# Performance work log

Measured on AMD Instinct MI355X. Metric: run time of the kernel, lower is better.

The kernel has to match this reference:

```python
import math
import jax, jax.numpy as jnp
import numpy as np

FS = 16000          # sample rate implied by undefined global `fs` in source
NFFT = 320          # win_len == frame_len
HOP = 160           # inc
C_SOUND = 340.0
ARRAY_DIS = 0.027


def _steering(F, n_ch, angle_deg):
    # h = conj(exp(-1j*2*pi*f_k * sensor * d * sin(theta)/c)) -> exp(+1j*...)
    f_k = np.arange(F) * (FS // NFFT)                      # integer bins * 50 Hz
    delay = np.arange(n_ch) * ARRAY_DIS * np.sin(angle_deg * np.pi / 180.0) / C_SOUND
    h = np.exp(1j * 2.0 * np.pi * f_k[:, None] * delay[None, :]).astype(np.complex64)
    return jnp.asarray(h)[..., None]                       # [F, C, 1]


def _stft(x, window):
    # x: [B, C, L] float32; torch.stft defaults: center=True, reflect pad
    pad = NFFT // 2
    xp = jnp.pad(x, ((0, 0), (0, 0), (pad, pad)), mode='reflect')
    T = 1 + (xp.shape[-1] - NFFT) // HOP
    idx = jnp.arange(T)[:, None] * HOP + jnp.arange(NFFT)[None, :]
    frames = xp[:, :, idx] * window                        # [B, C, T, NFFT]
    return jnp.fft.rfft(frames, axis=-1)                   # [B, C, T, F] complex64


def _istft(S):
    # S: [B, F, T] complex; torch.istft with default (rectangular) window
    frames = jnp.fft.irfft(jnp.moveaxis(S, 1, 2), n=NFFT, axis=-1)  # [B, T, NFFT]
    B, T, _ = frames.shape
    out_len = NFFT + HOP * (T - 1)
    idx = jnp.arange(T)[:, None] * HOP + jnp.arange(NFFT)[None, :]
    out = jnp.zeros((B, out_len), frames.dtype).at[:, idx].add(frames)
    wsum = jnp.zeros((out_len,), frames.dtype).at[idx.reshape(-1)].add(1.0)
    pad = NFFT // 2
    return (out / wsum)[:, pad:-pad]


def setup_inputs() -> dict:
    key = jax.random.key(0)
    B, L, C = 8, 160000, 4
    mc_wav = jax.random.normal(key, (B, L, C), dtype=jnp.float32)
    # torch.kaiser_window(320, periodic=True, beta=6)
    window = jnp.asarray(np.kaiser(NFFT + 1, 6.0)[:NFFT].astype(np.float32))
    return {"mc_wav": mc_wav, "window": window}


def reference(mc_wav, window):
    B, L, C = mc_wav.shape
    # pre-normalize: remove DC per channel, scale by per-batch global max-abs
    x = mc_wav - jnp.mean(mc_wav, axis=1, keepdims=True)
    x = x / jnp.max(jnp.abs(x), axis=(1, 2), keepdims=True)
    x = jnp.transpose(x, (0, 2, 1))                        # [B, C, L]

    S = _stft(x, window)                                   # [B, C, T, F]
    F = S.shape[-1]
    Xs = jnp.transpose(S, (2, 0, 3, 1))                    # [T, B, F, C] frames-first
    T = Xs.shape[0]

    h1 = _steering(F, C, -40.0)                            # [F, C, 1]
    h2 = _steering(F, C, 40.0)
    eye = jnp.eye(C, dtype=S.dtype)

    def beam(invR, h, X):
        num = jnp.einsum('bfcd,fdo->bfco', invR, h)        # invR @ h  [B,F,C,1]
        den = jnp.einsum('fco,bfco->bf', h.conj(), num)    # h^H invR h
        w = num[..., 0] / den[..., None]                   # [B, F, C]
        return jnp.einsum('bfc,bfc->bf', w.conj(), X)      # w^H X

    def step(RXX, inp):
        X, first = inp                                     # X: [B, F, C]
        outer = jnp.einsum('bfc,bfd->bfcd', X, X.conj())
        RXX = jnp.where(first, outer, 0.05 * RXX + 0.95 * outer)
        tr = jnp.trace(RXX, axis1=-2, axis2=-1)[..., None, None]
        invR = jnp.linalg.inv(RXX + (tr / C) * eye)        # diag-loaded inverse
        return RXX, (beam(invR, h1, X), beam(invR, h2, X))

    RXX0 = jnp.zeros((B, F, C, C), dtype=S.dtype)
    firsts = jnp.arange(T) == 0
    _, (s1, s2) = jax.lax.scan(step, RXX0, (Xs, firsts))

    S1 = jnp.transpose(s1, (1, 2, 0))                      # [B, F, T]
    S2 = jnp.transpose(s2, (1, 2, 0))
    return _istft(S1), _istft(S2)
```

## Files before the change

kernel.cpp:

```cpp
#include <hip/hip_runtime.h>
#include <hip/hip_bf16.h>
#include <math.h>

#define BB 8
#define LL 160000
#define CC 4
#define NFFT 320
#define HOP 160
#define FB 161
#define TT 1001
#define TP 1024
#define RBLK 128
#define PI_D 3.14159265358979323846
#define NPAD 160320

#define SCH 504
#define KWARM 4

#define GM 16016
#define KSEC 352
#define LDK 704
#define KT 11

typedef __attribute__((ext_vector_type(8))) short bf16x8;
typedef __attribute__((ext_vector_type(4))) float f32x4;

__device__ __forceinline__ void ldsdma16(const short* g, short* l){
    __builtin_amdgcn_global_load_lds((const __attribute__((address_space(1))) void*)g,
                                     (__attribute__((address_space(3))) void*)l, 16, 0, 0);
}

__device__ __forceinline__ float2 cmulf(float2 a, float2 b){
    return make_float2(a.x*b.x - a.y*b.y, a.x*b.y + a.y*b.x);
}
__device__ __forceinline__ float2 cmulcj(float2 a, float2 b){
    return make_float2(a.x*b.x + a.y*b.y, a.y*b.x - a.x*b.y);
}
__device__ __forceinline__ float2 cjmul(float2 a, float2 b){
    return make_float2(a.x*b.x + a.y*b.y, a.x*b.y - a.y*b.x);
}
__device__ __forceinline__ float2 csub(float2 a, float2 b){ return make_float2(a.x-b.x, a.y-b.y); }
__device__ __forceinline__ float2 cscale(float2 a, float s){ return make_float2(a.x*s, a.y*s); }
__device__ __forceinline__ float2 cdivf(float2 a, float2 b){
    float inv = 1.0f/(b.x*b.x + b.y*b.y);
    return make_float2((a.x*b.x + a.y*b.y)*inv, (a.y*b.x - a.x*b.y)*inv);
}
__device__ __forceinline__ short bf_hi(float v){
    __hip_bfloat16 h = __float2bfloat16(v);
    short s; __builtin_memcpy(&s, &h, 2); return s;
}
__device__ __forceinline__ short bf_lo(float v){
    __hip_bfloat16 h = __float2bfloat16(v);
    float r = v - __bfloat162float(h);
    __hip_bfloat16 l = __float2bfloat16(r);
    short s; __builtin_memcpy(&s, &l, 2); return s;
}

__global__ void k_gen(const float* __restrict__ win, float* __restrict__ htab,
                      short* __restrict__ Bts, short* __restrict__ Bt){
    int gid = blockIdx.x*256 + threadIdx.x;
    if (gid < 2*FB*CC){
        int i = gid;
        int c = i & 3;
        int k = (i >> 2) % FB;
        int m = i / (FB*CC);
        double coef = 2.0*PI_D*50.0*0.027*sin(40.0*PI_D/180.0)/340.0;
        double sgn = (m == 0) ? -1.0 : 1.0;
        double ph = sgn*coef*(double)k*(double)c;
        double s, c2;
        sincos(ph, &s, &c2);
        ((float2*)htab)[i] = make_float2((float)c2, (float)s);
        return;
    }
    gid -= 2*FB*CC;
    if (gid < 384*640){
        int col = gid / 640, kk = gid % 640;
        int n = (kk >= 320) ? kk - 320 : kk;
        int sec = (kk >= 320) ? 1 : 0;
        float v = 0.f;
        if (col < 2*FB){
            int k = col >> 1;
            double th = 2.0*PI_D*(double)k*(double)n/320.0;
            double s, co; sincos(th, &s, &co);
            double tw = (col & 1) ? -s : co;
            v = (float)((double)win[n]*tw);
        }
        Bts[gid] = sec ? bf_lo(v) : bf_hi(v);
        return;
    }
    gid -= 384*640;
    if (gid < NFFT*LDK){
        int n = gid / LDK, kk = gid % LDK;
        int sec = (kk >= KSEC) ? 1 : 0;
        int kk2 = kk - (sec ? KSEC : 0);
        float v = 0.f;
        if (kk2 < 2*FB){
            int bin = kk2 >> 1;
            double c = ((bin == 0 || bin == 160) ? 1.0 : 2.0) / 320.0;
            double th = 2.0*PI_D*(double)bin*(double)n/320.0;
            double s, co; sincos(th, &s, &co);
            v = (float)((kk2 & 1) ? -c*s : c*co);
        }
        Bt[(size_t)n*LDK + kk] = sec ? bf_lo(v) : bf_hi(v);
    }
}

__global__ __launch_bounds__(256) void k_stats1(const float* __restrict__ in, float* __restrict__ part){
    __shared__ float4 s4[256];
    __shared__ float4 mn4[256];
    __shared__ float4 mx4[256];
    int b = blockIdx.x / RBLK, chunk = blockIdx.x % RBLK;
    int tid = threadIdx.x;
    const float4* p = (const float4*)(in + (size_t)b*LL*CC);
    const int per = LL / RBLK;
    int start = chunk*per;
    float4 s  = make_float4(0.f,0.f,0.f,0.f);
    float4 mn = make_float4( 3.4e38f, 3.4e38f, 3.4e38f, 3.4e38f);
    float4 mx = make_float4(-3.4e38f,-3.4e38f,-3.4e38f,-3.4e38f);
    for (int i = start + tid; i < start + per; i += 256){
        float4 v = p[i];
        s.x += v.x; s.y += v.y; s.z += v.z; s.w += v.w;
        mn.x = fminf(mn.x, v.x); mn.y = fminf(mn.y, v.y); mn.z = fminf(mn.z, v.z); mn.w = fminf(mn.w, v.w);
        mx.x = fmaxf(mx.x, v.x); mx.y = fmaxf(mx.y, v.y); mx.z = fmaxf(mx.z, v.z); mx.w = fmaxf(mx.w, v.w);
    }
    s4[tid] = s; mn4[tid] = mn; mx4[tid] = mx;
    __syncthreads();
    for (int st = 128; st >= 1; st >>= 1){
        if (tid < st){
            float4 a = s4[tid], c = s4[tid+st];
            s4[tid] = make_float4(a.x+c.x, a.y+c.y, a.z+c.z, a.w+c.w);
            float4 d = mn4[tid], e = mn4[tid+st];
            mn4[tid] = make_float4(fminf(d.x,e.x), fminf(d.y,e.y), fminf(d.z,e.z), fminf(d.w,e.w));
            float4 f = mx4[tid], g = mx4[tid+st];
            mx4[tid] = make_float4(fmaxf(f.x,g.x), fmaxf(f.y,g.y), fmaxf(f.z,g.z), fmaxf(f.w,g.w));
        }
        __syncthreads();
    }
    if (tid == 0){
        float* dst = part + (size_t)(b*RBLK + chunk)*12;
        float4 a = s4[0], d = mn4[0], f = mx4[0];
        dst[0]=a.x; dst[1]=a.y; dst[2]=a.z; dst[3]=a.w;
        dst[4]=d.x; dst[5]=d.y; dst[6]=d.z; dst[7]=d.w;
        dst[8]=f.x; dst[9]=f.y; dst[10]=f.z; dst[11]=f.w;
    }
}

__global__ __launch_bounds__(128) void k_stats2(const float* __restrict__ part,
                                                float* __restrict__ mean, float* __restrict__ invmax){
    __shared__ float4 s4[128];
    __shared__ float4 mn4[128];
    __shared__ float4 mx4[128];
    int b = blockIdx.x, tid = threadIdx.x;
    const float* src = part + (size_t)(b*RBLK + tid)*12;
    s4[tid]  = make_float4(src[0], src[1], src[2], src[3]);
    mn4[tid] = make_float4(src[4], src[5], src[6], src[7]);
    mx4[tid] = make_float4(src[8], src[9], src[10], src[11]);
    __syncthreads();
    for (int st = 64; st >= 1; st >>= 1){
        if (tid < st){
            float4 a = s4[tid], c = s4[tid+st];
            s4[tid] = make_float4(a.x+c.x, a.y+c.y, a.z+c.z, a.w+c.w);
            float4 d = mn4[tid], e = mn4[tid+st];
            mn4[tid] = make_float4(fminf(d.x,e.x), fminf(d.y,e.y), fminf(d.z,e.z), fminf(d.w,e.w));
            float4 f = mx4[tid], g = mx4[tid+st];
            mx4[tid] = make_float4(fmaxf(f.x,g.x), fmaxf(f.y,g.y), fmaxf(f.z,g.z), fmaxf(f.w,g.w));
        }
        __syncthreads();
    }
    if (tid == 0){
        float4 sum = s4[0], mn = mn4[0], mx = mx4[0];
        float m0 = sum.x*(1.0f/LL), m1 = sum.y*(1.0f/LL), m2 = sum.z*(1.0f/LL), m3 = sum.w*(1.0f/LL);
        mean[b*4+0]=m0; mean[b*4+1]=m1; mean[b*4+2]=m2; mean[b*4+3]=m3;
        float a0 = fmaxf(mx.x - m0, m0 - mn.x);
        float a1 = fmaxf(mx.y - m1, m1 - mn.y);
        float a2 = fmaxf(mx.z - m2, m2 - mn.z);
        float a3 = fmaxf(mx.w - m3, m3 - mn.w);
        invmax[b] = 1.0f / fmaxf(fmaxf(a0, a1), fmaxf(a2, a3));
    }
}

__global__ __launch_bounds__(256) void k_anorm(const float* __restrict__ in,
        const float* __restrict__ mean, const float* __restrict__ invmax,
        short* __restrict__ Ahi, short* __restrict__ Alo){
    int gid = blockIdx.x*256 + threadIdx.x;
    if (gid >= BB*CC*(NPAD/8)) return;
    int p8 = gid % (NPAD/8);
    int bc = gid / (NPAD/8);
    int b = bc >> 2;
    float mc = mean[bc];
    float iv = invmax[b];
    const float* px = in + (size_t)b*LL*CC + (bc & 3);
    bf16x8 h8, l8;
    #pragma unroll
    for (int j = 0; j < 8; ++j){
        int p = p8*8 + j - 160;
        int m2 = p < 0 ? -p : (p >= LL ? 2*LL - 2 - p : p);
        float v = (px[(size_t)m2*CC] - mc) * iv;
        __hip_bfloat16 h = __float2bfloat16(v);
        float r = v - __bfloat162float(h);
        __hip_bfloat16 l = __float2bfloat16(r);
        short hs, ls; __builtin_memcpy(&hs, &h, 2); __builtin_memcpy(&ls, &l, 2);
        h8[j] = hs; l8[j] = ls;
    }
    size_t o = (size_t)bc*NPAD + (size_t)p8*8;
    *(bf16x8*)&Ahi[o] = h8;
    *(bf16x8*)&Alo[o] = l8;
}

__global__ __launch_bounds__(256) void k_gstft(const short* __restrict__ Ahi, const short* __restrict__ Alo,
        const short* __restrict__ Bts, float* __restrict__ S){
    __shared__ short stage[16384];
    float* Ct = (float*)stage;
    int tid = threadIdx.x;
    int row0 = blockIdx.x*64;
    int col0 = blockIdx.y*64;
    int b  = row0 >> 12;
    int t0 = (row0 & 4095) >> 2;
    if (t0 >= TT) return;
    int wave = tid >> 6, lane = tid & 63;
    int wm = wave >> 1, wn = wave & 1;
    int l15 = lane & 15, quad = lane >> 4;
    int rowS  = wave*16 + (lane >> 2);
    int chunk = (lane & 3) ^ ((lane >> 3) & 3);
    int tls = t0 + (rowS >> 2); if (tls >= TT) tls = TT - 1;
    size_t gao = (size_t)(b*4 + (rowS & 3))*NPAD + (size_t)tls*160 + chunk*8;
    const short* gAh = Ahi + gao;
    const short* gAl = Alo + gao;
    const short* gB  = Bts + (size_t)(col0 + rowS)*640 + chunk*8;
    short* lA = stage + wave*512;
    int sw  = (l15 >> 1) & 3;
    int c0r = (quad ^ sw) * 8;
    int ra0 = (wm*32 + l15)*32 + c0r;
    int ra1 = (wm*32 + 16 + l15)*32 + c0r;
    int rb0 = (wn*32 + l15)*32 + c0r;
    int rb1 = (wn*32 + 16 + l15)*32 + c0r;
    f32x4 acc00 = {0.f,0.f,0.f,0.f}, acc01 = acc00, acc10 = acc00, acc11 = acc00;

    #define STG(kt_, off_) do{ \
        ldsdma16(gAh + (kt_)*32,       lA + (off_));        \
        ldsdma16(gAl + (kt_)*32,       lA + (off_) + 2048); \
        ldsdma16(gB  + (kt_)*32,       lA + (off_) + 4096); \
        ldsdma16(gB  + (kt_)*32 + 320, lA + (off_) + 6144); \
    }while(0)

    STG(0, 0);
    STG(1, 8192);
    #pragma unroll
    for (int kt = 0; kt < 10; ++kt){
        int offc = (kt & 1) ? 8192 : 0;
        if (kt < 9) asm volatile("s_waitcnt vmcnt(4)" ::: "memory");
        else        asm volatile("s_waitcnt vmcnt(0)" ::: "memory");
        __builtin_amdgcn_s_barrier();
        bf16x8 a0h = *(bf16x8*)&stage[offc + ra0];
        bf16x8 a1h = *(bf16x8*)&stage[offc + ra1];
        bf16x8 a0l = *(bf16x8*)&stage[offc + 2048 + ra0];
        bf16x8 a1l = *(bf16x8*)&stage[offc + 2048 + ra1];
        bf16x8 b0h = *(bf16x8*)&stage[offc + 4096 + rb0];
        bf16x8 b1h = *(bf16x8*)&stage[offc + 4096 + rb1];
        bf16x8 b0l = *(bf16x8*)&stage[offc + 6144 + rb0];
        bf16x8 b1l = *(bf16x8*)&stage[offc + 6144 + rb1];
        asm volatile("s_waitcnt lgkmcnt(0)" ::: "memory");
        __builtin_amdgcn_sched_barrier(0);
        __builtin_amdgcn_s_barrier();
        if (kt < 8) STG(kt+2, offc);
        acc00 = __builtin_amdgcn_mfma_f32_16x16x32_bf16(a0h, b0h, acc00, 0, 0, 0);
        acc01 = __builtin_amdgcn_mfma_f32_16x16x32_bf16(a0h, b1h, acc01, 0, 0, 0);
        acc10 = __builtin_amdgcn_mfma_f32_16x16x32_bf16(a1h, b0h, acc10, 0, 0, 0);
        acc11 = __builtin_amdgcn_mfma_f32_16x16x32_bf16(a1h, b1h, acc11, 0, 0, 0);
        acc00 = __builtin_amdgcn_mfma_f32_16x16x32_bf16(a0l, b0h, acc00, 0, 0, 0);
        acc01 = __builtin_amdgcn_mfma_f32_16x16x32_bf16(a0l, b1h, acc01, 0, 0, 0);
        acc10 = __builtin_amdgcn_mfma_f32_16x16x32_bf16(a1l, b0h, acc10, 0, 0, 0);
        acc11 = __builtin_amdgcn_mfma_f32_16x16x32_bf16(a1l, b1h, acc11, 0, 0, 0);
        acc00 = __builtin_amdgcn_mfma_f32_16x16x32_bf16(a0h, b0l, acc00, 0, 0, 0);
        acc01 = __builtin_amdgcn_mfma_f32_16x16x32_bf16(a0h, b1l, acc01, 0, 0, 0);
        acc10 = __builtin_amdgcn_mfma_f32_16x16x32_bf16(a1h, b0l, acc10, 0, 0, 0);
        acc11 = __builtin_amdgcn_mfma_f32_16x16x32_bf16(a1h, b1l, acc11, 0, 0, 0);
    }
    #undef STG
    #pragma unroll
    for (int r = 0; r < 4; ++r){
        int rl = wm*32 + quad*4 + r;
        Ct[rl*66 + wn*32 + l15]           = acc00[r];
        Ct[rl*66 + wn*32 + l15 + 16]      = acc01[r];
        Ct[(rl+16)*66 + wn*32 + l15]      = acc10[r];
        Ct[(rl+16)*66 + wn*32 + l15 + 16] = acc11[r];
    }
    __syncthreads();
    int tl = tid & 15, h = (tid >> 4) & 1, kq = tid >> 5;
    int t = t0 + tl;
    if (t < TT){
        float4* S4 = (float4*)S;
        for (int kk = kq; kk < 32; kk += 8){
            int kg = (col0 >> 1) + kk;
            if (kg < FB){
                float2 e0 = *(float2*)&Ct[(tl*4 + 2*h)*66 + 2*kk];
                float2 e1 = *(float2*)&Ct[(tl*4 + 2*h + 1)*66 + 2*kk];
                S4[((size_t)(b*FB + kg)*TT + t)*2 + h] = make_float4(e0.x, e0.y, e1.x, e1.y);
            }
        }
    }
}

#define UPD(first) do{ \
    float aa = (first) ? 0.f : 0.05f; float wg = (first) ? 1.f : 0.95f; \
    float y0x=wg*x0.x, y0y=wg*x0.y, y1x=wg*x1.x, y1y=wg*x1.y; \
    float y2x=wg*x2.x, y2y=wg*x2.y, y3x=wg*x3.x, y3y=wg*x3.y; \
    d0 = aa*d0 + y0x*x0.x + y0y*x0.y; \
    d1 = aa*d1 + y1x*x1.x + y1y*x1.y; \
    d2 = aa*d2 + y2x*x2.x + y2y*x2.y; \
    d3 = aa*d3 + y3x*x3.x + y3y*x3.y; \
    r10.x = aa*r10.x + y1x*x0.x + y1y*x0.y;  r10.y = aa*r10.y + y1y*x0.x - y1x*x0.y; \
    r20.x = aa*r20.x + y2x*x0.x + y2y*x0.y;  r20.y = aa*r20.y + y2y*x0.x - y2x*x0.y; \
    r30.x = aa*r30.x + y3x*x0.x + y3y*x0.y;  r30.y = aa*r30.y + y3y*x0.x - y3x*x0.y; \
    r21.x = aa*r21.x + y2x*x1.x + y2y*x1.y;  r21.y = aa*r21.y + y2y*x1.x - y2x*x1.y; \
    r31.x = aa*r31.x + y3x*x1.x + y3y*x1.y;  r31.y = aa*r31.y + y3y*x1.x - y3x*x1.y; \
    r32.x = aa*r32.x + y3x*x2.x + y3y*x2.y;  r32.y = aa*r32.y + y3y*x2.x - y3x*x2.y; \
}while(0)

__global__ __launch_bounds__(512) void k_scan(const float* __restrict__ S, const float* __restrict__ htab,
                      float* __restrict__ S1, float* __restrict__ S2){
    __shared__ float4 tile[1008];
    int bid = blockIdx.x;
    int half = bid & 1;
    int bf = bid >> 1;
    int f  = bf % FB;
    int tid = threadIdx.x;
    int tbase = half*SCH;
    int te  = tbase + SCH; if (te > TT) te = TT;
    int nst = 2*(te - tbase);
    const float4* Sg = (const float4*)S + (size_t)bf*TT*2;
    const float4* Sp = Sg + (size_t)tbase*2;
    for (int i = tid; i < nst; i += 512)
        tile[i ^ ((i>>4)&7)] = Sp[i];
    __syncthreads();
    float2 out1, out2;
    int t0 = tbase + tid;
    bool act = (tid < SCH) && (t0 < TT);
    if (act){
        const float2* hp = (const float2*)htab;
        float2 ha0 = hp[f*4+0], ha1 = hp[f*4+1], ha2 = hp[f*4+2], ha3 = hp[f*4+3];
        float2 hb0 = hp[(FB+f)*4+0], hb1 = hp[(FB+f)*4+1], hb2 = hp[(FB+f)*4+2], hb3 = hp[(FB+f)*4+3];
        float d0=0,d1=0,d2=0,d3=0;
        float2 r10={0,0}, r20={0,0}, r30={0,0}, r21={0,0}, r31={0,0}, r32={0,0};
        int ts = t0 - KWARM; if (ts < 0) ts = 0;
        for (int tau = ts; tau < t0; ++tau){
            float4 v0, v1;
            if (tau >= tbase){
                int i0 = 2*(tau - tbase);
                v0 = tile[i0 ^ ((i0>>4)&7)];
                v1 = tile[(i0+1) ^ ((i0>>4)&7)];
            } else {
                v0 = Sg[2*tau];
                v1 = Sg[2*tau + 1];
            }
            float2 x0 = make_float2(v0.x, v0.y), x1 = make_float2(v0.z, v0.w);
            float2 x2 = make_float2(v1.x, v1.y), x3 = make_float2(v1.z, v1.w);
            UPD(tau == 0);
        }
        {
            int t = t0;
            int i0 = 2*(t - tbase);
            float4 v0 = tile[i0 ^ ((i0>>4)&7)];
            float4 v1 = tile[(i0+1) ^ ((i0>>4)&7)];
            float2 x0 = make_float2(v0.x, v0.y), x1 = make_float2(v0.z, v0.w);
            float2 x2 = make_float2(v1.x, v1.y), x3 = make_float2(v1.z, v1.w);
            UPD(t == 0);
            float trc = d0 + d1 + d2 + d3;
            float lam = trc * 0.25f;
            float e0 = d0 + lam, e1 = d1 + lam, e2 = d2 + lam, e3 = d3 + lam;
            float detP = e0*e1 - (r10.x*r10.x + r10.y*r10.y);
            float2 w00 = csub(cscale(r20, e1), cmulf(r10, r21));
            float2 w01 = csub(cscale(r30, e1), cmulf(r10, r31));
            float2 w10 = csub(cscale(r21, e0), cjmul(r10, r20));
            float2 w11 = csub(cscale(r31, e0), cjmul(r10, r30));
            float2 va = cjmul(r30, w00), vb = cjmul(r31, w10);
            float2 V10 = make_float2(va.x + vb.x, -(va.y + vb.y));
            float reV00 = r20.x*w00.x + r20.y*w00.y + r21.x*w10.x + r21.y*w10.y;
            float reV11 = r30.x*w01.x + r30.y*w01.y + r31.x*w11.x + r31.y*w11.y;
            float t00 = detP*e2 - reV00;
            float t11 = detP*e3 - reV11;
            float2 t10 = csub(cscale(r32, detP), V10);
            float detT = t00*t11 - (t10.x*t10.x + t10.y*t10.y);
            #pragma unroll
            for (int m = 0; m < 2; ++m){
                float2 h0 = m ? hb0 : ha0;
                float2 h1 = m ? hb1 : ha1;
                float2 h2 = m ? hb2 : ha2;
                float2 h3 = m ? hb3 : ha3;
                float2 g0 = csub(cscale(h0, e1), cjmul(r10, h1));
                float2 g1 = csub(cscale(h1, e0), cmulf(r10, h0));
                float2 ta = cmulf(r20, g0), tb = cmulf(r21, g1);
                float2 hh0 = make_float2(detP*h2.x - ta.x - tb.x, detP*h2.y - ta.y - tb.y);
                ta = cmulf(r30, g0); tb = cmulf(r31, g1);
                float2 hh1 = make_float2(detP*h3.x - ta.x - tb.x, detP*h3.y - ta.y - tb.y);
                float2 y20 = csub(cscale(hh0, t11), cjmul(t10, hh1));
                float2 y21 = csub(cscale(hh1, t00), cmulf(t10, hh0));
                float2 u20 = cscale(y20, detP), u21 = cscale(y21, detP);
                ta = cmulcj(y20, r20); tb = cmulcj(y21, r30);
                float2 q0 = make_float2(detT*h0.x - ta.x - tb.x, detT*h0.y - ta.y - tb.y);
                ta = cmulcj(y20, r21); tb = cmulcj(y21, r31);
                float2 q1 = make_float2(detT*h1.x - ta.x - tb.x, detT*h1.y - ta.y - tb.y);
                float2 u10 = csub(cscale(q0, e1), cjmul(r10, q1));
                float2 u11 = csub(cscale(q1, e0), cmulf(r10, q0));
                float2 den = cjmul(h0, u10), tmp;
                tmp = cjmul(h1, u11); den.x += tmp.x; den.y += tmp.y;
                tmp = cjmul(h2, u20); den.x += tmp.x; den.y += tmp.y;
                tmp = cjmul(h3, u21); den.x += tmp.x; den.y += tmp.y;
                float2 num = cjmul(u10, x0);
                tmp = cjmul(u11, x1); num.x += tmp.x; num.y += tmp.y;
                tmp = cjmul(u20, x2); num.x += tmp.x; num.y += tmp.y;
                tmp = cjmul(u21, x3); num.x += tmp.x; num.y += tmp.y;
                float2 s = cdivf(num, make_float2(den.x, -den.y));
                if (m) out2 = s; else out1 = s;
            }
        }
    }
    __syncthreads();
    float2* o1 = (float2*)tile;
    float2* o2 = ((float2*)tile) + 528;
    if (act){
        int lt = t0 - tbase;
        int iw = lt ^ ((lt>>3)&7);
        o1[iw] = out1;
        o2[iw] = out2;
    }
    __syncthreads();
    int nout = te - tbase;
    float2* S1g = (float2*)S1 + (size_t)bf*TT + tbase;
    float2* S2g = (float2*)S2 + (size_t)bf*TT + tbase;
    for (int i = tid; i < nout; i += 512){
        int ir = i ^ ((i>>3)&7);
        S1g[i] = o1[ir];
        S2g[i] = o2[ir];
    }
}

__global__ __launch_bounds__(256) void k_pack(const float* __restrict__ S1, const float* __restrict__ S2,
                                              short* __restrict__ A){
    __shared__ short tile[32*708];
    int bid = blockIdx.x;
    int tb = bid & 31, rb = bid >> 5;
    int t0 = tb*32;
    int beam = rb >> 3, b = rb & 7;
    const float2* Sp = (const float2*)(beam ? S2 : S1) + (size_t)b*FB*TT;
    int tid = threadIdx.x;
    for (int idx = tid; idx < 32*176; idx += 256){
        int bin = idx >> 5, tq = idx & 31;
        int t = t0 + tq;
        float2 s = make_float2(0.f, 0.f);
        if (bin < FB && t < TT) s = Sp[(size_t)bin*TT + t];
        int c0 = 2*bin;
        tile[tq*708 + c0]            = bf_hi(s.x);
        tile[tq*708 + c0 + 1]        = bf_hi(s.y);
        tile[tq*708 + KSEC + c0]     = bf_lo(s.x);
        tile[tq*708 + KSEC + c0 + 1] = bf_lo(s.y);
    }
    __syncthreads();
    for (int idx = tid; idx < 32*176; idx += 256){
        int tq = idx / 176, k4 = idx % 176;
        int t = t0 + tq;
        if (t < TT)
            *(short4*)&A[(size_t)(rb*TT + t)*LDK + k4*4] = *(short4*)&tile[tq*708 + k4*4];
    }
}

__global__ __launch_bounds__(256) void k_gemm(const short* __restrict__ A, const short* __restrict__ Bt,
                                              float* __restrict__ C){
    __shared__ short sb2[8192];
    int tid = threadIdx.x;
    int row0 = blockIdx.x * 64;
    int col0 = blockIdx.y * 64;
    int wave = tid >> 6, lane = tid & 63;
    int wm = wave >> 1, wn = wave & 1;
    int l15 = lane & 15, quad = lane >> 4;
    int rowS  = wave*16 + (lane >> 2);
    int chunk = (lane & 3) ^ ((lane >> 3) & 3);
    int grS = row0 + rowS; if (grS >= GM) grS = GM - 1;
    const short* gA = A  + (size_t)grS*LDK + chunk*8;
    const short* gB = Bt + (size_t)(col0 + rowS)*LDK + chunk*8;
    short* lA = sb2 + wave*512;
    int sw  = (l15 >> 1) & 3;
    int c0r = (quad ^ sw) * 8;
    int ra0 = (wm*32 + l15)*32 + c0r;
    int ra1 = (wm*32 + 16 + l15)*32 + c0r;
    int rb0 = (wn*32 + l15)*32 + c0r;
    int rb1 = (wn*32 + 16 + l15)*32 + c0r;
    f32x4 acc00 = {0.f,0.f,0.f,0.f}, acc01 = acc00, acc10 = acc00, acc11 = acc00;

    #define KOF(s_, ka_, kb_) { int sg_ = ((s_) >= 22) ? 2 : ((s_) >= 11) ? 1 : 0; \
        int kt_ = (s_) - sg_*11; \
        ka_ = ((sg_ == 1) ? KSEC : 0) + kt_*32; \
        kb_ = ((sg_ == 2) ? KSEC : 0) + kt_*32; }
    #define STG2(s_, off_) do{ int ka_, kb_; KOF(s_, ka_, kb_); \
        ldsdma16(gA + ka_, lA + (off_));        \
        ldsdma16(gB + kb_, lA + (off_) + 2048); \
    }while(0)

    STG2(0, 0);
    STG2(1, 4096);
    #pragma unroll
    for (int s = 0; s < 33; ++s){
        int offc = (s & 1) ? 4096 : 0;
        if (s < 32) asm volatile("s_waitcnt vmcnt(2)" ::: "memory");
        else        asm volatile("s_waitcnt vmcnt(0)" ::: "memory");
        __builtin_amdgcn_s_barrier();
        bf16x8 a0 = *(bf16x8*)&sb2[offc + ra0];
        bf16x8 a1 = *(bf16x8*)&sb2[offc + ra1];
        bf16x8 b0 = *(bf16x8*)&sb2[offc + 2048 + rb0];
        bf16x8 b1 = *(bf16x8*)&sb2[offc + 2048 + rb1];
        asm volatile("s_waitcnt lgkmcnt(0)" ::: "memory");
        __builtin_amdgcn_sched_barrier(0);
        __builtin_amdgcn_s_barrier();
        if (s < 31) STG2(s+2, offc);
        acc00 = __builtin_amdgcn_mfma_f32_16x16x32_bf16(a0, b0, acc00, 0, 0, 0);
        acc01 = __builtin_amdgcn_mfma_f32_16x16x32_bf16(a0, b1, acc01, 0, 0, 0);
        acc10 = __builtin_amdgcn_mfma_f32_16x16x32_bf16(a1, b0, acc10, 0, 0, 0);
        acc11 = __builtin_amdgcn_mfma_f32_16x16x32_bf16(a1, b1, acc11, 0, 0, 0);
    }
    #undef STG2
    #undef KOF
    for (int r = 0; r < 4; ++r){
        int orow0 = row0 + wm*32 + quad*4 + r;
        int ocol0 = col0 + wn*32 + l15;
        if (orow0 < GM){
            C[(size_t)orow0*NFFT + ocol0]      = acc00[r];
            C[(size_t)orow0*NFFT + ocol0 + 16] = acc01[r];
        }
        if (orow0 + 16 < GM){
            C[(size_t)(orow0+16)*NFFT + ocol0]      = acc10[r];
            C[(size_t)(orow0+16)*NFFT + ocol0 + 16] = acc11[r];
        }
    }
}

__global__ __launch_bounds__(256) void k_ola(const float* __restrict__ frames, float* __restrict__ out){
    int gid = blockIdx.x*256 + threadIdx.x;
    if (gid >= 2*BB*(LL/4)) return;
    int o4 = (gid % (LL/4))*4;
    int rb = gid / (LL/4);
    int i  = o4 + HOP;
    int t1 = i / HOP;
    int r  = i - t1*HOP;
    const float4* fb = (const float4*)(frames + (size_t)rb*TT*NFFT);
    float4 a = fb[(t1*NFFT + r) >> 2];
    float4 b = fb[((t1-1)*NFFT + r + HOP) >> 2];
    ((float4*)out)[gid] = make_float4(0.5f*(a.x+b.x), 0.5f*(a.y+b.y), 0.5f*(a.z+b.z), 0.5f*(a.w+b.w));
}

extern "C" void kernel_launch(void* const* d_in, const int* in_sizes, int n_in,
                              void* d_out, int out_size, void* d_ws, size_t ws_size,
                              hipStream_t stream){
    const float* in  = (const float*)d_in[0];
    const float* win = (const float*)d_in[1];
    float* ws = (float*)d_ws;
    float* mean   = ws;
    float* invmax = ws + 32;
    float* htab   = ws + 48;
    float* S1     = ws + 3072;
    size_t nS1 = (size_t)2*BB*FB*TT;
    float* S2 = S1 + nS1;
    float* S  = S2 + nS1;
    float* part = S1;
    short* Ahi = (short*)S1;
    short* Alo = Ahi + (size_t)BB*CC*NPAD;
    short* Bts = (short*)d_out;
    short* Bt  = (short*)((float*)d_out + 131072);
    short* A  = (short*)S;
    float* frames = S1;

    int ngen = 2*FB*CC + 384*640 + NFFT*LDK;
    k_gen<<<dim3((ngen + 255)/256), dim3(256), 0, stream>>>(win, htab, Bts, Bt);
    k_stats1<<<dim3(BB*RBLK), dim3(256), 0, stream>>>(in, part);
    k_stats2<<<dim3(BB), dim3(128), 0, stream>>>(part, mean, invmax);
    k_anorm<<<dim3((BB*CC*(NPAD/8) + 255)/256), dim3(256), 0, stream>>>(in, mean, invmax, Ahi, Alo);
    k_gstft<<<dim3(BB*TP*CC/64, 6), dim3(256), 0, stream>>>(Ahi, Alo, Bts, S);
    k_scan<<<dim3(2*BB*FB), dim3(512), 0, stream>>>(S, htab, S1, S2);
    k_pack<<<dim3(512), dim3(256), 0, stream>>>(S1, S2, A);
    k_gemm<<<dim3((GM + 63)/64, NFFT/64), dim3(256), 0, stream>>>(A, Bt, frames);
    k_ola<<<dim3((2*BB*(LL/4) + 255)/256), dim3(256), 0, stream>>>(frames, (float*)d_out);
}
```

Measured before the change: 220.4 us.

## Enlarge STFT and iSTFT GEMM tiles to 128x128 with 512-thread blocks

Both MFMA GEMM kernels move from 64x64 tiles with 4 waves to 128x128 tiles with 8 waves, so each wave now computes a 32x64 sub-tile with 8 accumulators. This is meant to raise operand reuse per LDS load and cut global traffic. The STFT epilogue drops the LDS transpose and writes straight from registers using lane shuffles, and the layout of S changes to split channel pairs into separate planes, so the scan kernel's loads are rewritten to match. The cost is more registers per thread, fewer blocks, and wasted work on padded columns (320 is not a multiple of 128), which needs bounds guards.

```diff
diff --git a/kernel.cpp b/kernel.cpp
--- a/kernel.cpp
+++ b/kernel.cpp
@@ -207,16 +207,14 @@
     *(bf16x8*)&Alo[o] = l8;
 }
 
-__global__ __launch_bounds__(256) void k_gstft(const short* __restrict__ Ahi, const short* __restrict__ Alo,
+__global__ __launch_bounds__(512, 4) void k_gstft(const short* __restrict__ Ahi, const short* __restrict__ Alo,
         const short* __restrict__ Bts, float* __restrict__ S){
-    __shared__ short stage[16384];
-    float* Ct = (float*)stage;
+    __shared__ short stage[32768];
     int tid = threadIdx.x;
-    int row0 = blockIdx.x*64;
-    int col0 = blockIdx.y*64;
+    int row0 = blockIdx.x*128;
+    int col0 = blockIdx.y*128;
     int b  = row0 >> 12;
     int t0 = (row0 & 4095) >> 2;
-    if (t0 >= TT) return;
     int wave = tid >> 6, lane = tid & 63;
     int wm = wave >> 1, wn = wave & 1;
     int l15 = lane & 15, quad = lane >> 4;
@@ -231,74 +229,87 @@
     int sw  = (l15 >> 1) & 3;
     int c0r = (quad ^ sw) * 8;
     int ra0 = (wm*32 + l15)*32 + c0r;
-    int ra1 = (wm*32 + 16 + l15)*32 + c0r;
-    int rb0 = (wn*32 + l15)*32 + c0r;
-    int rb1 = (wn*32 + 16 + l15)*32 + c0r;
-    f32x4 acc00 = {0.f,0.f,0.f,0.f}, acc01 = acc00, acc10 = acc00, acc11 = acc00;
+    int rb0 = (wn*64 + l15)*32 + c0r;
+    f32x4 c00 = {0.f,0.f,0.f,0.f}, c01 = c00, c02 = c00, c03 = c00;
+    f32x4 c10 = c00, c11 = c00, c12 = c00, c13 = c00;
 
     #define STG(kt_, off_) do{ \
-        ldsdma16(gAh + (kt_)*32,       lA + (off_));        \
-        ldsdma16(gAl + (kt_)*32,       lA + (off_) + 2048); \
-        ldsdma16(gB  + (kt_)*32,       lA + (off_) + 4096); \
-        ldsdma16(gB  + (kt_)*32 + 320, lA + (off_) + 6144); \
+        ldsdma16(gAh + (kt_)*32,       lA + (off_));         \
+        ldsdma16(gAl + (kt_)*32,       lA + (off_) + 4096);  \
+        ldsdma16(gB  + (kt_)*32,       lA + (off_) + 8192);  \
+        ldsdma16(gB  + (kt_)*32 + 320, lA + (off_) + 12288); \
     }while(0)
 
     STG(0, 0);
-    STG(1, 8192);
+    STG(1, 16384);
     #pragma unroll
     for (int kt = 0; kt < 10; ++kt){
-        int offc = (kt & 1) ? 8192 : 0;
+        int offc = (kt & 1) ? 16384 : 0;
         if (kt < 9) asm volatile("s_waitcnt vmcnt(4)" ::: "memory");
         else        asm volatile("s_waitcnt vmcnt(0)" ::: "memory");
         __builtin_amdgcn_s_barrier();
         bf16x8 a0h = *(bf16x8*)&stage[offc + ra0];
-        bf16x8 a1h = *(bf16x8*)&stage[offc + ra1];
-        bf16x8 a0l = *(bf16x8*)&stage[offc + 2048 + ra0];
-        bf16x8 a1l = *(bf16x8*)&stage[offc + 2048 + ra1];
-        bf16x8 b0h = *(bf16x8*)&stage[offc + 4096 + rb0];
-        bf16x8 b1h = *(bf16x8*)&stage[offc + 4096 + rb1];
-        bf16x8 b0l = *(bf16x8*)&stage[offc + 6144 + rb0];
-        bf16x8 b1l = *(bf16x8*)&stage[offc + 6144 + rb1];
+        bf16x8 a1h = *(bf16x8*)&stage[offc + ra0 + 512];
+        bf16x8 a0l = *(bf16x8*)&stage[offc + 4096 + ra0];
+        bf16x8 a1l = *(bf16x8*)&stage[offc + 4096 + ra0 + 512];
+        bf16x8 b0h = *(bf16x8*)&stage[offc + 8192 + rb0];
+        bf16x8 b1h = *(bf16x8*)&stage[offc + 8192 + rb0 + 512];
+        bf16x8 b2h = *(bf16x8*)&stage[offc + 8192 + rb0 + 1024];
+        bf16x8 b3h = *(bf16x8*)&stage[offc + 8192 + rb0 + 1536];
+        bf16x8 b0l = *(bf16x8*)&stage[offc + 12288 + rb0];
+        bf16x8 b1l = *(bf16x8*)&stage[offc + 12288 + rb0 + 512];
+        bf16x8 b2l = *(bf16x8*)&stage[offc + 12288 + rb0 + 1024];
+        bf16x8 b3l = *(bf16x8*)&stage[offc + 12288 + rb0 + 1536];
         asm volatile("s_waitcnt lgkmcnt(0)" ::: "memory");
         __builtin_amdgcn_sched_barrier(0);
         __builtin_amdgcn_s_barrier();
         if (kt < 8) STG(kt+2, offc);
-        acc00 = __builtin_amdgcn_mfma_f32_16x16x32_bf16(a0h, b0h, acc00, 0, 0, 0);
-        acc01 = __builtin_amdgcn_mfma_f32_16x16x32_bf16(a0h, b1h, acc01, 0, 0, 0);
-        acc10 = __builtin_amdgcn_mfma_f32_16x16x32_bf16(a1h, b0h, acc10, 0, 0, 0);
-        acc11 = __builtin_amdgcn_mfma_f32_16x16x32_bf16(a1h, b1h, acc11, 0, 0, 0);
-        acc00 = __builtin_amdgcn_mfma_f32_16x16x32_bf16(a0l, b0h, acc00, 0, 0, 0);
-        acc01 = __builtin_amdgcn_mfma_f32_16x16x32_bf16(a0l, b1h, acc01, 0, 0, 0);
-        acc10 = __builtin_amdgcn_mfma_f32_16x16x32_bf16(a1l, b0h, acc10, 0, 0, 0);
-        acc11 = __builtin_amdgcn_mfma_f32_16x16x32_bf16(a1l, b1h, acc11, 0, 0, 0);
-        acc00 = __builtin_amdgcn_mfma_f32_16x16x32_bf16(a0h, b0l, acc00, 0, 0, 0);
-        acc01 = __builtin_amdgcn_mfma_f32_16x16x32_bf16(a0h, b1l, acc01, 0, 0, 0);
-        acc10 = __builtin_amdgcn_mfma_f32_16x16x32_bf16(a1h, b0l, acc10, 0, 0, 0);
-        acc11 = __builtin_amdgcn_mfma_f32_16x16x32_bf16(a1h, b1l, acc11, 0, 0, 0);
+        c00 = __builtin_amdgcn_mfma_f32_16x16x32_bf16(a0h, b0h, c00, 0, 0, 0);
+        c01 = __builtin_amdgcn_mfma_f32_16x16x32_bf16(a0h, b1h, c01, 0, 0, 0);
+        c02 = __builtin_amdgcn_mfma_f32_16x16x32_bf16(a0h, b2h, c02, 0, 0, 0);
+        c03 = __builtin_amdgcn_mfma_f32_16x16x32_bf16(a0h, b3h, c03, 0, 0, 0);
+        c10 = __builtin_amdgcn_mfma_f32_16x16x32_bf16(a1h, b0h, c10, 0, 0, 0);
+        c11 = __builtin_amdgcn_mfma_f32_16x16x32_bf16(a1h, b1h, c11, 0, 0, 0);
+        c12 = __builtin_amdgcn_mfma_f32_16x16x32_bf16(a1h, b2h, c12, 0, 0, 0);
+        c13 = __builtin_amdgcn_mfma_f32_16x16x32_bf16(a1h, b3h, c13, 0, 0, 0);
+        c00 = __builtin_amdgcn_mfma_f32_16x16x32_bf16(a0l, b0h, c00, 0, 0, 0);
+        c01 = __builtin_amdgcn_mfma_f32_16x16x32_bf16(a0l, b1h, c01, 0, 0, 0);
+        c02 = __builtin_amdgcn_mfma_f32_16x16x32_bf16(a0l, b2h, c02, 0, 0, 0);
+        c03 = __builtin_amdgcn_mfma_f32_16x16x32_bf16(a0l, b3h, c03, 0, 0, 0);
+        c10 = __builtin_amdgcn_mfma_f32_16x16x32_bf16(a1l, b0h, c10, 0, 0, 0);
+        c11 = __builtin_amdgcn_mfma_f32_16x16x32_bf16(a1l, b1h, c11, 0, 0, 0);
+        c12 = __builtin_amdgcn_mfma_f32_16x16x32_bf16(a1l, b2h, c12, 0, 0, 0);
+        c13 = __builtin_amdgcn_mfma_f32_16x16x32_bf16(a1l, b3h, c13, 0, 0, 0);
+        c00 = __builtin_amdgcn_mfma_f32_16x16x32_bf16(a0h, b0l, c00, 0, 0, 0);
+        c01 = __builtin_amdgcn_mfma_f32_16x16x32_bf16(a0h, b1l, c01, 0, 0, 0);
+        c02 = __builtin_amdgcn_mfma_f32_16x16x32_bf16(a0h, b2l, c02, 0, 0, 0);
+        c03 = __builtin_amdgcn_mfma_f32_16x16x32_bf16(a0h, b3l, c03, 0, 0, 0);
+        c10 = __builtin_amdgcn_mfma_f32_16x16x32_bf16(a1h, b0l, c10, 0, 0, 0);
+        c11 = __builtin_amdgcn_mfma_f32_16x16x32_bf16(a1h, b1l, c11, 0, 0, 0);
+        c12 = __builtin_amdgcn_mfma_f32_16x16x32_bf16(a1h, b2l, c12, 0, 0, 0);
+        c13 = __builtin_amdgcn_mfma_f32_16x16x32_bf16(a1h, b3l, c13, 0, 0, 0);
     }
     #undef STG
-    #pragma unroll
-    for (int r = 0; r < 4; ++r){
-        int rl = wm*32 + quad*4 + r;
-        Ct[rl*66 + wn*32 + l15]           = acc00[r];
-        Ct[rl*66 + wn*32 + l15 + 16]      = acc01[r];
-        Ct[(rl+16)*66 + wn*32 + l15]      = acc10[r];
-        Ct[(rl+16)*66 + wn*32 + l15 + 16] = acc11[r];
-    }
-    __syncthreads();
-    int tl = tid & 15, h = (tid >> 4) & 1, kq = tid >> 5;
-    int t = t0 + tl;
-    if (t < TT){
-        float4* S4 = (float4*)S;
-        for (int kk = kq; kk < 32; kk += 8){
-            int kg = (col0 >> 1) + kk;
-            if (kg < FB){
-                float2 e0 = *(float2*)&Ct[(tl*4 + 2*h)*66 + 2*kk];
-                float2 e1 = *(float2*)&Ct[(tl*4 + 2*h + 1)*66 + 2*kk];
-                S4[((size_t)(b*FB + kg)*TT + t)*2 + h] = make_float4(e0.x, e0.y, e1.x, e1.y);
-            }
-        }
-    }
+    int tq  = t0 + wm*8 + quad;
+    int kgb = (col0 >> 1) + wn*32 + (l15 >> 1);
+    int h   = l15 & 1;
+    float4* S4 = (float4*)S;
+    #define EPI(cf, i_, j_) do{ \
+        int t = tq + 4*(i_); \
+        int kg = kgb + 8*(j_); \
+        if (t < TT && kg < FB){ \
+            float p0 = __shfl_xor(cf[0], 1); \
+            float p1 = __shfl_xor(cf[1], 1); \
+            float p2 = __shfl_xor(cf[2], 1); \
+            float p3 = __shfl_xor(cf[3], 1); \
+            float4 v = h ? make_float4(p2, cf[2], p3, cf[3]) \
+                         : make_float4(cf[0], p0, cf[1], p1); \
+            S4[((size_t)((b*FB + kg)*2 + h))*TT + t] = v; \
+        } \
+    }while(0)
+    EPI(c00, 0, 0); EPI(c01, 0, 1); EPI(c02, 0, 2); EPI(c03, 0, 3);
+    EPI(c10, 1, 0); EPI(c11, 1, 1); EPI(c12, 1, 2); EPI(c13, 1, 3);
+    #undef EPI
 }
 
 #define UPD(first) do{ \
@@ -328,10 +339,12 @@
     int tbase = half*SCH;
     int te  = tbase + SCH; if (te > TT) te = TT;
     int nst = 2*(te - tbase);
-    const float4* Sg = (const float4*)S + (size_t)bf*TT*2;
-    const float4* Sp = Sg + (size_t)tbase*2;
-    for (int i = tid; i < nst; i += 512)
-        tile[i ^ ((i>>4)&7)] = Sp[i];
+    const float4* P0 = (const float4*)S + (size_t)(bf*2)*TT;
+    const float4* P1 = P0 + TT;
+    for (int i = tid; i < nst; i += 512){
+        int tt = tbase + (i >> 1);
+        tile[i ^ ((i>>4)&7)] = (i & 1) ? P1[tt] : P0[tt];
+    }
     __syncthreads();
     float2 out1, out2;
     int t0 = tbase + tid;
@@ -350,8 +363,8 @@
                 v0 = tile[i0 ^ ((i0>>4)&7)];
                 v1 = tile[(i0+1) ^ ((i0>>4)&7)];
             } else {
-                v0 = Sg[2*tau];
-                v1 = Sg[2*tau + 1];
+                v0 = P0[tau];
+                v1 = P1[tau];
             }
             float2 x0 = make_float2(v0.x, v0.y), x1 = make_float2(v0.z, v0.w);
             float2 x2 = make_float2(v1.x, v1.y), x3 = make_float2(v1.z, v1.w);
@@ -464,28 +477,28 @@
     }
 }
 
-__global__ __launch_bounds__(256) void k_gemm(const short* __restrict__ A, const short* __restrict__ Bt,
-                                              float* __restrict__ C){
-    __shared__ short sb2[8192];
+__global__ __launch_bounds__(512, 4) void k_gemm(const short* __restrict__ A, const short* __restrict__ Bt,
+                                                 float* __restrict__ C){
+    __shared__ short sb2[16384];
     int tid = threadIdx.x;
-    int row0 = blockIdx.x * 64;
-    int col0 = blockIdx.y * 64;
+    int row0 = blockIdx.x * 128;
+    int col0 = blockIdx.y * 128;
     int wave = tid >> 6, lane = tid & 63;
     int wm = wave >> 1, wn = wave & 1;
     int l15 = lane & 15, quad = lane >> 4;
     int rowS  = wave*16 + (lane >> 2);
     int chunk = (lane & 3) ^ ((lane >> 3) & 3);
     int grS = row0 + rowS; if (grS >= GM) grS = GM - 1;
+    int grB = col0 + rowS; if (grB >= NFFT) grB = NFFT - 1;
     const short* gA = A  + (size_t)grS*LDK + chunk*8;
-    const short* gB = Bt + (size_t)(col0 + rowS)*LDK + chunk*8;
+    const short* gB = Bt + (size_t)grB*LDK + chunk*8;
     short* lA = sb2 + wave*512;
     int sw  = (l15 >> 1) & 3;
     int c0r = (quad ^ sw) * 8;
     int ra0 = (wm*32 + l15)*32 + c0r;
-    int ra1 = (wm*32 + 16 + l15)*32 + c0r;
-    int rb0 = (wn*32 + l15)*32 + c0r;
-    int rb1 = (wn*32 + 16 + l15)*32 + c0r;
-    f32x4 acc00 = {0.f,0.f,0.f,0.f}, acc01 = acc00, acc10 = acc00, acc11 = acc00;
+    int rb0 = (wn*64 + l15)*32 + c0r;
+    f32x4 c00 = {0.f,0.f,0.f,0.f}, c01 = c00, c02 = c00, c03 = c00;
+    f32x4 c10 = c00, c11 = c00, c12 = c00, c13 = c00;
 
     #define KOF(s_, ka_, kb_) { int sg_ = ((s_) >= 22) ? 2 : ((s_) >= 11) ? 1 : 0; \
         int kt_ = (s_) - sg_*11; \
@@ -493,42 +506,53 @@
         kb_ = ((sg_ == 2) ? KSEC : 0) + kt_*32; }
     #define STG2(s_, off_) do{ int ka_, kb_; KOF(s_, ka_, kb_); \
         ldsdma16(gA + ka_, lA + (off_));        \
-        ldsdma16(gB + kb_, lA + (off_) + 2048); \
+        ldsdma16(gB + kb_, lA + (off_) + 4096); \
     }while(0)
 
     STG2(0, 0);
-    STG2(1, 4096);
+    STG2(1, 8192);
     #pragma unroll
     for (int s = 0; s < 33; ++s){
-        int offc = (s & 1) ? 4096 : 0;
+        int offc = (s & 1) ? 8192 : 0;
         if (s < 32) asm volatile("s_waitcnt vmcnt(2)" ::: "memory");
         else        asm volatile("s_waitcnt vmcnt(0)" ::: "memory");
         __builtin_amdgcn_s_barrier();
         bf16x8 a0 = *(bf16x8*)&sb2[offc + ra0];
-        bf16x8 a1 = *(bf16x8*)&sb2[offc + ra1];
-        bf16x8 b0 = *(bf16x8*)&sb2[offc + 2048 + rb0];
-        bf16x8 b1 = *(bf16x8*)&sb2[offc + 2048 + rb1];
+        bf16x8 a1 = *(bf16x8*)&sb2[offc + ra0 + 512];
+        bf16x8 b0 = *(bf16x8*)&sb2[offc + 4096 + rb0];
+        bf16x8 b1 = *(bf16x8*)&sb2[offc + 4096 + rb0 + 512];
+        bf16x8 b2 = *(bf16x8*)&sb2[offc + 4096 + rb0 + 1024];
+        bf16x8 b3 = *(bf16x8*)&sb2[offc + 4096 + rb0 + 1536];
         asm volatile("s_waitcnt lgkmcnt(0)" ::: "memory");
         __builtin_amdgcn_sched_barrier(0);
         __builtin_amdgcn_s_barrier();
         if (s < 31) STG2(s+2, offc);
-        acc00 = __builtin_amdgcn_mfma_f32_16x16x32_bf16(a0, b0, acc00, 0, 0, 0);
-        acc01 = __builtin_amdgcn_mfma_f32_16x16x32_bf16(a0, b1, acc01, 0, 0, 0);
-        acc10 = __builtin_amdgcn_mfma_f32_16x16x32_bf16(a1, b0, acc10, 0, 0, 0);
-        acc11 = __builtin_amdgcn_mfma_f32_16x16x32_bf16(a1, b1, acc11, 0, 0, 0);
+        c00 = __builtin_amdgcn_mfma_f32_16x16x32_bf16(a0, b0, c00, 0, 0, 0);
+        c01 = __builtin_amdgcn_mfma_f32_16x16x32_bf16(a0, b1, c01, 0, 0, 0);
+        c02 = __builtin_amdgcn_mfma_f32_16x16x32_bf16(a0, b2, c02, 0, 0, 0);
+        c03 = __builtin_amdgcn_mfma_f32_16x16x32_bf16(a0, b3, c03, 0, 0, 0);
+        c10 = __builtin_amdgcn_mfma_f32_16x16x32_bf16(a1, b0, c10, 0, 0, 0);
+        c11 = __builtin_amdgcn_mfma_f32_16x16x32_bf16(a1, b1, c11, 0, 0, 0);
+        c12 = __builtin_amdgcn_mfma_f32_16x16x32_bf16(a1, b2, c12, 0, 0, 0);
+        c13 = __builtin_amdgcn_mfma_f32_16x16x32_bf16(a1, b3, c13, 0, 0, 0);
     }
     #undef STG2
     #undef KOF
+    #pragma unroll
     for (int r = 0; r < 4; ++r){
         int orow0 = row0 + wm*32 + quad*4 + r;
-        int ocol0 = col0 + wn*32 + l15;
+        int oc = col0 + wn*64 + l15;
         if (orow0 < GM){
-            C[(size_t)orow0*NFFT + ocol0]      = acc00[r];
-            C[(size_t)orow0*NFFT + ocol0 + 16] = acc01[r];
+            if (oc      < NFFT) C[(size_t)orow0*NFFT + oc]      = c00[r];
+            if (oc + 16 < NFFT) C[(size_t)orow0*NFFT + oc + 16] = c01[r];
+            if (oc + 32 < NFFT) C[(size_t)orow0*NFFT + oc + 32] = c02[r];
+            if (oc + 48 < NFFT) C[(size_t)orow0*NFFT + oc + 48] = c03[r];
         }
         if (orow0 + 16 < GM){
-            C[(size_t)(orow0+16)*NFFT + ocol0]      = acc10[r];
-            C[(size_t)(orow0+16)*NFFT + ocol0 + 16] = acc11[r];
+            if (oc      < NFFT) C[(size_t)(orow0+16)*NFFT + oc]      = c10[r];
+            if (oc + 16 < NFFT) C[(size_t)(orow0+16)*NFFT + oc + 16] = c11[r];
+            if (oc + 32 < NFFT) C[(size_t)(orow0+16)*NFFT + oc + 32] = c12[r];
+            if (oc + 48 < NFFT) C[(size_t)(orow0+16)*NFFT + oc + 48] = c13[r];
         }
     }
 }
@@ -573,9 +597,9 @@
     k_stats1<<<dim3(BB*RBLK), dim3(256), 0, stream>>>(in, part);
     k_stats2<<<dim3(BB), dim3(128), 0, stream>>>(part, mean, invmax);
     k_anorm<<<dim3((BB*CC*(NPAD/8) + 255)/256), dim3(256), 0, stream>>>(in, mean, invmax, Ahi, Alo);
-    k_gstft<<<dim3(BB*TP*CC/64, 6), dim3(256), 0, stream>>>(Ahi, Alo, Bts, S);
+    k_gstft<<<dim3(BB*TP*CC/128, 3), dim3(512), 0, stream>>>(Ahi, Alo, Bts, S);
     k_scan<<<dim3(2*BB*FB), dim3(512), 0, stream>>>(S, htab, S1, S2);
     k_pack<<<dim3(512), dim3(256), 0, stream>>>(S1, S2, A);
-    k_gemm<<<dim3((GM + 63)/64, NFFT/64), dim3(256), 0, stream>>>(A, Bt, frames);
+    k_gemm<<<dim3((GM + 127)/128, (NFFT + 127)/128), dim3(512), 0, stream>>>(A, Bt, frames);
     k_ola<<<dim3((2*BB*(LL/4) + 255)/256), dim3(256), 0, stream>>>(frames, (float*)d_out);
 }
```

Result: faster. 209.5 us (-5.0%).
